# Kernel optimization log

Measured on AMD Instinct MI355X. Metric: run time of the kernel, lower is better.

The kernel has to match this reference:

```python
import jax, jax.numpy as jnp
import numpy as np

B, S, D, H = 8, 2048, 1024, 8
HD = D // H


def _linear_params(key, d_in, d_out):
    kw, kb = jax.random.split(key)
    w = jax.random.normal(kw, (d_out, d_in), jnp.float32) * 0.02
    b = jax.random.normal(kb, (d_out,), jnp.float32) * 0.02
    return w, b


def setup_inputs() -> dict:
    key = jax.random.key(0)
    ks = jax.random.split(key, 16)
    inp = {}
    inp['input_seq'] = jax.random.normal(ks[0], (B, S, D), jnp.float32)
    inp['output_seq'] = jax.random.normal(ks[1], (B, S, D), jnp.float32)
    # PositionalEncoding parameter: sin(arange(D) / 10000 ** (arange(D)/D))
    ar = jnp.arange(D, dtype=jnp.float32)
    inp['pe'] = jnp.sin(ar / 10000.0 ** (ar / D))
    names = ['enc_wq enc_bq', 'enc_wk enc_bk', 'enc_wv enc_bv',
             'enc_w1 enc_b1', 'enc_w2 enc_b2',
             'dec_s_wq dec_s_bq', 'dec_s_wk dec_s_bk', 'dec_s_wv dec_s_bv',
             'dec_c_wq dec_c_bq', 'dec_c_wk dec_c_bk', 'dec_c_wv dec_c_bv',
             'dec_w1 dec_b1', 'dec_w2 dec_b2', 'fc_w fc_b']
    for i, pair in enumerate(names):
        wn, bn = pair.split()
        w, b = _linear_params(ks[2 + i], D, D)
        inp[wn], inp[bn] = w, b
    return inp


def _mha(q_in, k_in, wq, bq, wk, bk, wv, bv):
    # Faithful to source: head split WITHOUT transpose -> per-position 8x8 head mixing.
    q = (q_in @ wq.T + bq).reshape(q_in.shape[0], q_in.shape[1], H, HD)
    k = (k_in @ wk.T + bk).reshape(k_in.shape[0], k_in.shape[1], H, HD)
    v = (k_in @ wv.T + bv).reshape(k_in.shape[0], k_in.shape[1], H, HD)
    scores = jnp.einsum('bsih,bsjh->bsij', q, k) / jnp.sqrt(jnp.float32(HD))
    w = jax.nn.softmax(scores, axis=-1)  # dropout before softmax is identity at eval
    out = jnp.einsum('bsij,bsjh->bsih', w, v)
    return out.reshape(q_in.shape[0], q_in.shape[1], -1)


def reference(input_seq, output_seq, pe,
              enc_wq, enc_bq, enc_wk, enc_bk, enc_wv, enc_bv,
              enc_w1, enc_b1, enc_w2, enc_b2,
              dec_s_wq, dec_s_bq, dec_s_wk, dec_s_bk, dec_s_wv, dec_s_bv,
              dec_c_wq, dec_c_bq, dec_c_wk, dec_c_bk, dec_c_wv, dec_c_bv,
              dec_w1, dec_b1, dec_w2, dec_b2, fc_w, fc_b):
    x = input_seq + pe  # additive positional encoding
    # encoder layer
    a = _mha(x, x, enc_wq, enc_bq, enc_wk, enc_bk, enc_wv, enc_bv)
    enc_out = jax.nn.relu(a @ enc_w1.T + enc_b1) @ enc_w2.T + enc_b2
    # decoder layer (training branch: output_seq given)
    sa = _mha(output_seq, output_seq, dec_s_wq, dec_s_bq, dec_s_wk, dec_s_bk, dec_s_wv, dec_s_bv)
    ca = _mha(sa, enc_out, dec_c_wq, dec_c_bq, dec_c_wk, dec_c_bk, dec_c_wv, dec_c_bv)
    dec_out = jax.nn.relu(ca @ dec_w1.T + dec_b1) @ dec_w2.T + dec_b2
    return dec_out @ fc_w.T + fc_b
```

## Files before the change

kernel.cpp:

```cpp
#include <hip/hip_runtime.h>
#include <stdint.h>


#define TOKENS 16384
#define DMODEL 1024

typedef unsigned short ushort_t;
typedef __attribute__((ext_vector_type(8))) short short8;
typedef __attribute__((ext_vector_type(4))) float floatx4;

__device__ __forceinline__ float b2f(ushort_t u) {
  union { uint32_t i; float f; } v; v.i = ((uint32_t)u) << 16; return v.f;
}
__device__ __forceinline__ ushort_t f2b(float f) {
  union { float f; uint32_t i; } v; v.f = f;
  uint32_t r = v.i + 0x7fffu + ((v.i >> 16) & 1u);
  return (ushort_t)(r >> 16);
}

__device__ __forceinline__ void pack8(const float* __restrict__ g, ushort_t* dst) {
  float4 x = *(const float4*)g;
  float4 y = *(const float4*)(g + 4);
  ushort_t o[8] = {f2b(x.x), f2b(x.y), f2b(x.z), f2b(x.w),
                   f2b(y.x), f2b(y.y), f2b(y.z), f2b(y.w)};
  *(uint4*)dst = *(uint4*)o;
}

#define GLD16(g, l)                                                          \
  __builtin_amdgcn_global_load_lds(                                          \
      (const __attribute__((address_space(1))) void*)(g),                    \
      (__attribute__((address_space(3))) void*)(l), 16, 0, 0)

struct ConvArgs {
  const float* src[14];
  ushort_t* dst[14];
};

__global__ __launch_bounds__(256) void conv_w_kernel(ConvArgs a) {
  const int w = blockIdx.y;
  const int idx = (blockIdx.x * 256 + threadIdx.x) * 8;
  pack8(a.src[w] + idx, a.dst[w] + idx);
}

__global__ __launch_bounds__(256) void conv_x_kernel(
    const float* __restrict__ src, ushort_t* __restrict__ dst) {
  const int idx = (blockIdx.x * 256 + threadIdx.x) * 8;
  pack8(src + idx, dst + idx);
}

__global__ __launch_bounds__(256) void add_pe_kernel(
    const float* __restrict__ in, const float* __restrict__ pe,
    ushort_t* __restrict__ out) {
  int idx = (blockIdx.x * 256 + threadIdx.x) * 8;
  int d = idx & (DMODEL - 1);
  float4 a0 = *(const float4*)(in + idx);
  float4 a1 = *(const float4*)(in + idx + 4);
  float4 p0 = *(const float4*)(pe + d);
  float4 p1 = *(const float4*)(pe + d + 4);
  ushort_t o[8] = {f2b(a0.x + p0.x), f2b(a0.y + p0.y), f2b(a0.z + p0.z), f2b(a0.w + p0.w),
                   f2b(a1.x + p1.x), f2b(a1.y + p1.y), f2b(a1.z + p1.z), f2b(a1.w + p1.w)};
  *(uint4*)(out + idx) = *(uint4*)o;
}

__device__ __forceinline__ void load_af(const ushort_t* p, int aoff, int cs0,
                                        int cs1, short8 (&af)[4][2]) {
  p += aoff;
#pragma unroll
  for (int i = 0; i < 4; i++) {
    af[i][0] = *(const short8*)&p[i * 1024 + cs0];
    af[i][1] = *(const short8*)&p[i * 1024 + cs1];
  }
}

__device__ __forceinline__ void load_bf(const ushort_t* p, int boff, int cs0,
                                        int cs1, short8 (&bf)[2][2]) {
  p += boff;
#pragma unroll
  for (int j = 0; j < 2; j++) {
    bf[j][0] = *(const short8*)&p[j * 1024 + cs0];
    bf[j][1] = *(const short8*)&p[j * 1024 + cs1];
  }
}

template <int QA, int QB>
__device__ __forceinline__ void mfma_region(floatx4 (&acc)[4][4][2],
                                            const short8 (&af)[4][2],
                                            const short8 (&b0)[2][2],
                                            const short8 (&b1)[2][2]) {
  __builtin_amdgcn_s_setprio(1);
#pragma unroll
  for (int i = 0; i < 4; i++)
#pragma unroll
    for (int j = 0; j < 2; j++) {
      acc[QA][i][j] = __builtin_amdgcn_mfma_f32_16x16x32_bf16(
          af[i][0], b0[j][0], acc[QA][i][j], 0, 0, 0);
      acc[QA][i][j] = __builtin_amdgcn_mfma_f32_16x16x32_bf16(
          af[i][1], b0[j][1], acc[QA][i][j], 0, 0, 0);
    }
#pragma unroll
  for (int i = 0; i < 4; i++)
#pragma unroll
    for (int j = 0; j < 2; j++) {
      acc[QB][i][j] = __builtin_amdgcn_mfma_f32_16x16x32_bf16(
          af[i][0], b1[j][0], acc[QB][i][j], 0, 0, 0);
      acc[QB][i][j] = __builtin_amdgcn_mfma_f32_16x16x32_bf16(
          af[i][1], b1[j][1], acc[QB][i][j], 0, 0, 0);
    }
  __builtin_amdgcn_s_setprio(0);
}

#define BARSB asm volatile("s_barrier" ::: "memory")

#define STAGE_A4(dst, tk)                                                    \
  do {                                                                       \
    GLD16(gA + (size_t)(tk) * 64, (dst) + lo);                               \
    GLD16(gA + (size_t)(tk) * 64 + 65536, (dst) + 4096 + lo);                \
    GLD16(gA + (size_t)(tk) * 64 + 131072, (dst) + 8192 + lo);               \
    GLD16(gA + (size_t)(tk) * 64 + 196608, (dst) + 12288 + lo);              \
  } while (0)
#define STAGE_B4(dst, tk)                                                    \
  do {                                                                       \
    GLD16(gB + (size_t)(tk) * 64, (dst) + lo);                               \
    GLD16(gB + (size_t)(tk) * 64 + 65536, (dst) + 4096 + lo);                \
    GLD16(gB + (size_t)(tk) * 64 + 131072, (dst) + 8192 + lo);               \
    GLD16(gB + (size_t)(tk) * 64 + 196608, (dst) + 12288 + lo);              \
  } while (0)

template <bool RELU, bool OUT32>
__global__ __launch_bounds__(512, 2) void gemm_bt(
    const ushort_t* __restrict__ A, const ushort_t* __restrict__ W,
    const float* __restrict__ bias, void* __restrict__ Cp) {
  constexpr int K = 1024, N = 1024, NT = 16;
  extern __shared__ ushort_t smem[];
  ushort_t* sA = smem;
  ushort_t* sB = smem + 49152;

  const int tid = threadIdx.x;
  const int lane = tid & 63;
  const int wid = tid >> 6;

  const int orig = blockIdx.x;
  const int swz = (orig & 7) * 32 + (orig >> 3);
  const int m0 = (swz >> 2) * 256;
  const int n0 = (swz & 3) * 256;

  const int qm = (wid >> 2) * 64;
  const int qn = (wid & 3) * 32;
  const int lr = lane & 15;
  const int lq = lane >> 4;
  const int xr = lane & 7;
  const int cs0 = (lq ^ xr) * 8;
  const int cs1 = ((4 + lq) ^ xr) * 8;
  const int aoff = (qm + lr) * 64;
  const int boff = (qn + lr) * 64;

  const int rl = tid >> 3;
  const int j8 = tid & 7;
  const int co = (j8 ^ (rl & 7)) * 8;
  const int lo = tid * 8;
  const ushort_t* gA = A + (size_t)(m0 + rl) * K + co;
  const ushort_t* gB = W + (size_t)(n0 + rl) * K + co;

  floatx4 acc[4][4][2] = {};
  short8 af[4][2], bf0[2][2], bf1[2][2];

  STAGE_A4(sA, 0);
  STAGE_B4(sB, 0);
  STAGE_A4(sA + 16384, 1);
  asm volatile("s_waitcnt vmcnt(4)" ::: "memory");
  BARSB;

  int ba = 0;
#pragma unroll 1
  for (int t = 0; t < NT; ++t) {
    const ushort_t* sAb = sA + ba * 16384;
    const ushort_t* sBb = sB + (t & 1) * 16384;
    int ba2 = ba + 2; if (ba2 >= 3) ba2 -= 3;
    ushort_t* sAs = sA + ba2 * 16384;
    ushort_t* sBs = sB + ((t + 1) & 1) * 16384;

    if (t + 1 < NT) STAGE_B4(sBs, t + 1);
    if (t + 2 < NT) STAGE_A4(sAs, t + 2);

    load_af(sAb, aoff, cs0, cs1, af);
    load_bf(sBb, boff, cs0, cs1, bf0);
    load_bf(sBb + 8192, boff, cs0, cs1, bf1);
    mfma_region<0, 1>(acc, af, bf0, bf1);
    load_af(sAb + 8192, aoff, cs0, cs1, af);
    mfma_region<2, 3>(acc, af, bf0, bf1);

    if (t + 2 < NT)
      asm volatile("s_waitcnt vmcnt(4)" ::: "memory");
    else
      asm volatile("s_waitcnt vmcnt(0)" ::: "memory");
    BARSB;

    ba = (ba == 2) ? 0 : ba + 1;
  }

  const int rbase = lq * 4;

  if constexpr (OUT32) {
    float* sCf = (float*)smem;
#pragma unroll
    for (int p = 0; p < 4; p++) {
      if ((qm >> 6) == (p & 1)) {
#pragma unroll
        for (int Nh = 0; Nh < 2; Nh++)
#pragma unroll
          for (int j = 0; j < 2; j++) {
            const int col = Nh * 128 + qn + j * 16 + lr;
            const float bv = bias[n0 + col];
#pragma unroll
            for (int i = 0; i < 4; i++)
#pragma unroll
              for (int r = 0; r < 4; r++) {
                float v = acc[(p >> 1) * 2 + Nh][i][j][r] + bv;
                if (RELU) v = fmaxf(v, 0.0f);
                sCf[(i * 16 + rbase + r) * 260 + col] = v;
              }
          }
      }
      __syncthreads();
#pragma unroll
      for (int u = 0; u < 8; u++) {
        const int lin = u * 512 + tid;
        const int row = lin >> 6;
        const int c4 = (lin & 63) * 4;
        *(float4*)((float*)Cp + (size_t)(m0 + p * 64 + row) * N + n0 + c4) =
            *(const float4*)&sCf[row * 260 + c4];
      }
      __syncthreads();
    }
    return;
  }

  ushort_t* sC = smem;
#pragma unroll
  for (int p = 0; p < 2; p++) {
#pragma unroll
    for (int Nh = 0; Nh < 2; Nh++)
#pragma unroll
      for (int j = 0; j < 2; j++) {
        const int col = Nh * 128 + qn + j * 16 + lr;
        const float bv = bias[n0 + col];
#pragma unroll
        for (int i = 0; i < 4; i++)
#pragma unroll
          for (int r = 0; r < 4; r++) {
            float v = acc[p * 2 + Nh][i][j][r] + bv;
            if (RELU) v = fmaxf(v, 0.0f);
            sC[(qm + i * 16 + rbase + r) * 264 + col] = f2b(v);
          }
      }
    __syncthreads();
#pragma unroll
    for (int u = 0; u < 8; u++) {
      const int lin = u * 512 + tid;
      const int row = lin >> 5;
      const int c8 = (lin & 31) * 8;
      *(uint4*)((ushort_t*)Cp + (size_t)(m0 + p * 128 + row) * N + n0 + c8) =
          *(const uint4*)&sC[row * 264 + c8];
    }
    __syncthreads();
  }
}

__global__ __launch_bounds__(256) void attn_kernel(
    const ushort_t* Q, const ushort_t* Kp, const ushort_t* Vp, ushort_t* O) {
  __shared__ __align__(16) ushort_t sq[4][1024];
  __shared__ __align__(16) ushort_t sk[4][1024];
  __shared__ __align__(16) ushort_t sv[4][1024];
  __shared__ float sp[4][64];

  const int t = threadIdx.x;
  const int w = t >> 6;
  const int lane = t & 63;
  const size_t base = ((size_t)blockIdx.x * 4 + w) * 1024;

  ((uint4*)sq[w])[lane] = ((const uint4*)(Q + base))[lane];
  ((uint4*)sq[w])[lane + 64] = ((const uint4*)(Q + base))[lane + 64];
  ((uint4*)sk[w])[lane] = ((const uint4*)(Kp + base))[lane];
  ((uint4*)sk[w])[lane + 64] = ((const uint4*)(Kp + base))[lane + 64];
  ((uint4*)sv[w])[lane] = ((const uint4*)(Vp + base))[lane];
  ((uint4*)sv[w])[lane + 64] = ((const uint4*)(Vp + base))[lane + 64];
  __syncthreads();

  {
    const int i = lane >> 3, j = lane & 7;
    const ushort_t* qr = &sq[w][i * 128];
    const ushort_t* kr = &sk[w][j * 128];
    float s = 0.0f;
#pragma unroll 16
    for (int h = 0; h < 128; h++) s += b2f(qr[h]) * b2f(kr[h]);
    s *= 0.08838834764831845f;
    float m = s;
#pragma unroll
    for (int off = 1; off < 8; off <<= 1) m = fmaxf(m, __shfl_xor(m, off, 64));
    float e = __expf(s - m);
    float sum = e;
#pragma unroll
    for (int off = 1; off < 8; off <<= 1) sum += __shfl_xor(sum, off, 64);
    sp[w][lane] = e / sum;
  }
  __syncthreads();

  {
    const int i = lane >> 3;
    const int hb = (lane & 7) * 16;
    float p[8];
#pragma unroll
    for (int jj = 0; jj < 8; jj++) p[jj] = sp[w][i * 8 + jj];
    float o[16];
#pragma unroll
    for (int h = 0; h < 16; h++) {
      float acc = 0.0f;
#pragma unroll
      for (int jj = 0; jj < 8; jj++) acc += p[jj] * b2f(sv[w][jj * 128 + hb + h]);
      o[h] = acc;
    }
    uint32_t packed[8];
#pragma unroll
    for (int u = 0; u < 8; u++)
      packed[u] = (uint32_t)f2b(o[2 * u]) | ((uint32_t)f2b(o[2 * u + 1]) << 16);
    uint4* dst = (uint4*)(O + base + i * 128 + hb);
    dst[0] = *(uint4*)&packed[0];
    dst[1] = *(uint4*)&packed[4];
  }
}

extern "C" void kernel_launch(void* const* d_in, const int* in_sizes, int n_in,
                              void* d_out, int out_size, void* d_ws, size_t ws_size,
                              hipStream_t stream) {
  const float* input_seq = (const float*)d_in[0];
  const float* output_seq = (const float*)d_in[1];
  const float* pe = (const float*)d_in[2];
  const float* wsrc[14] = {
      (const float*)d_in[3],  (const float*)d_in[5],  (const float*)d_in[7],
      (const float*)d_in[9],  (const float*)d_in[11], (const float*)d_in[13],
      (const float*)d_in[15], (const float*)d_in[17], (const float*)d_in[19],
      (const float*)d_in[21], (const float*)d_in[23], (const float*)d_in[25],
      (const float*)d_in[27], (const float*)d_in[29]};
  const float* enc_bq = (const float*)d_in[4];
  const float* enc_bk = (const float*)d_in[6];
  const float* enc_bv = (const float*)d_in[8];
  const float* enc_b1 = (const float*)d_in[10];
  const float* enc_b2 = (const float*)d_in[12];
  const float* dsq_b = (const float*)d_in[14];
  const float* dsk_b = (const float*)d_in[16];
  const float* dsv_b = (const float*)d_in[18];
  const float* dcq_b = (const float*)d_in[20];
  const float* dck_b = (const float*)d_in[22];
  const float* dcv_b = (const float*)d_in[24];
  const float* dec_b1 = (const float*)d_in[26];
  const float* dec_b2 = (const float*)d_in[28];
  const float* fc_b = (const float*)d_in[30];

  const size_t SZ = (size_t)TOKENS * DMODEL;
  const size_t WSZ = (size_t)DMODEL * DMODEL;
  ushort_t* bA = (ushort_t*)d_ws;
  ushort_t* bB = bA + SZ;
  ushort_t* oseq = bB + SZ;
  ushort_t* wts = oseq + SZ;
  ushort_t* oL = (ushort_t*)d_out;
  ushort_t* oH = oL + SZ;
  float* outf = (float*)d_out;

  static bool attr_set = false;
  if (!attr_set) {
    (void)hipFuncSetAttribute(reinterpret_cast<const void*>(&gemm_bt<false, false>),
                              hipFuncAttributeMaxDynamicSharedMemorySize, 163840);
    (void)hipFuncSetAttribute(reinterpret_cast<const void*>(&gemm_bt<true, false>),
                              hipFuncAttributeMaxDynamicSharedMemorySize, 163840);
    (void)hipFuncSetAttribute(reinterpret_cast<const void*>(&gemm_bt<false, true>),
                              hipFuncAttributeMaxDynamicSharedMemorySize, 163840);
    attr_set = true;
  }

  ConvArgs ca;
#pragma unroll
  for (int i = 0; i < 14; i++) { ca.src[i] = wsrc[i]; ca.dst[i] = wts + (size_t)i * WSZ; }

  const dim3 gG(TOKENS / 256 * (DMODEL / 256));
  const dim3 gblk(512);
  const dim3 blk(256);
  const int LDSB = 163840;
  const int gPE = TOKENS * DMODEL / (256 * 8);
  const int gAT = TOKENS / 4;

  conv_w_kernel<<<dim3(WSZ / (256 * 8), 14), blk, 0, stream>>>(ca);
  conv_x_kernel<<<gPE, blk, 0, stream>>>(output_seq, oseq);
  add_pe_kernel<<<gPE, blk, 0, stream>>>(input_seq, pe, bA);
  gemm_bt<false, false><<<gG, gblk, LDSB, stream>>>(bA, wts + 0 * WSZ, enc_bq, bB);
  gemm_bt<false, false><<<gG, gblk, LDSB, stream>>>(bA, wts + 1 * WSZ, enc_bk, oL);
  gemm_bt<false, false><<<gG, gblk, LDSB, stream>>>(bA, wts + 2 * WSZ, enc_bv, oH);
  attn_kernel<<<gAT, blk, 0, stream>>>(bB, oL, oH, bB);
  gemm_bt<true, false><<<gG, gblk, LDSB, stream>>>(bB, wts + 3 * WSZ, enc_b1, bA);
  gemm_bt<false, false><<<gG, gblk, LDSB, stream>>>(bA, wts + 4 * WSZ, enc_b2, bB);
  gemm_bt<false, false><<<gG, gblk, LDSB, stream>>>(oseq, wts + 5 * WSZ, dsq_b, bA);
  gemm_bt<false, false><<<gG, gblk, LDSB, stream>>>(oseq, wts + 6 * WSZ, dsk_b, oL);
  gemm_bt<false, false><<<gG, gblk, LDSB, stream>>>(oseq, wts + 7 * WSZ, dsv_b, oH);
  attn_kernel<<<gAT, blk, 0, stream>>>(bA, oL, oH, bA);
  gemm_bt<false, false><<<gG, gblk, LDSB, stream>>>(bA, wts + 8 * WSZ, dcq_b, oL);
  gemm_bt<false, false><<<gG, gblk, LDSB, stream>>>(bB, wts + 9 * WSZ, dck_b, oH);
  gemm_bt<false, false><<<gG, gblk, LDSB, stream>>>(bB, wts + 10 * WSZ, dcv_b, bA);
  attn_kernel<<<gAT, blk, 0, stream>>>(oL, oH, bA, oL);
  gemm_bt<true, false><<<gG, gblk, LDSB, stream>>>(oL, wts + 11 * WSZ, dec_b1, bB);
  gemm_bt<false, false><<<gG, gblk, LDSB, stream>>>(bB, wts + 12 * WSZ, dec_b2, bA);
  gemm_bt<false, true><<<gG, gblk, LDSB, stream>>>(bA, wts + 13 * WSZ, fc_b, outf);
}
```

Measured before the change: 845.0 us.

## Restructure GEMM main loop into 8-wave ping-pong schedule with double buffering

Replaces the triple-buffered A / double-buffered B pipeline with a double-buffered scheme. Each K tile is split into four quadrant MFMA phases separated by barriers, and LDS fragment loads and the next tile's global staging are interleaved between phases. The next tile's fragments are prefetched into alternating register sets. LDS use drops from 160KB to 128KB. The extra barriers per tile and the full vmcnt(0) wait could stall if global loads are not hidden, though the intent is tighter overlap of LDS reads with MFMA.

```diff
diff --git a/kernel.cpp b/kernel.cpp
--- a/kernel.cpp
+++ b/kernel.cpp
@@ -82,29 +82,18 @@
   }
 }
 
-template <int QA, int QB>
-__device__ __forceinline__ void mfma_region(floatx4 (&acc)[4][4][2],
-                                            const short8 (&af)[4][2],
-                                            const short8 (&b0)[2][2],
-                                            const short8 (&b1)[2][2]) {
+__device__ __forceinline__ void mfma_q(floatx4 (&accq)[4][2],
+                                       const short8 (&af)[4][2],
+                                       const short8 (&bf)[2][2]) {
   __builtin_amdgcn_s_setprio(1);
 #pragma unroll
   for (int i = 0; i < 4; i++)
 #pragma unroll
     for (int j = 0; j < 2; j++) {
-      acc[QA][i][j] = __builtin_amdgcn_mfma_f32_16x16x32_bf16(
-          af[i][0], b0[j][0], acc[QA][i][j], 0, 0, 0);
-      acc[QA][i][j] = __builtin_amdgcn_mfma_f32_16x16x32_bf16(
-          af[i][1], b0[j][1], acc[QA][i][j], 0, 0, 0);
-    }
-#pragma unroll
-  for (int i = 0; i < 4; i++)
-#pragma unroll
-    for (int j = 0; j < 2; j++) {
-      acc[QB][i][j] = __builtin_amdgcn_mfma_f32_16x16x32_bf16(
-          af[i][0], b1[j][0], acc[QB][i][j], 0, 0, 0);
-      acc[QB][i][j] = __builtin_amdgcn_mfma_f32_16x16x32_bf16(
-          af[i][1], b1[j][1], acc[QB][i][j], 0, 0, 0);
+      accq[i][j] = __builtin_amdgcn_mfma_f32_16x16x32_bf16(
+          af[i][0], bf[j][0], accq[i][j], 0, 0, 0);
+      accq[i][j] = __builtin_amdgcn_mfma_f32_16x16x32_bf16(
+          af[i][1], bf[j][1], accq[i][j], 0, 0, 0);
     }
   __builtin_amdgcn_s_setprio(0);
 }
@@ -126,6 +115,33 @@
     GLD16(gB + (size_t)(tk) * 64 + 196608, (dst) + 12288 + lo);              \
   } while (0)
 
+#define GROUP(tt, dd, b0c, b0n)                                              \
+  do {                                                                       \
+                                                                     \
+    if ((tt) + 1 < NT) {                                                     \
+      STAGE_A4(sA + ((dd) ^ 1) * 16384, (tt) + 1);                           \
+      STAGE_B4(sB + ((dd) ^ 1) * 16384, (tt) + 1);                           \
+    }                                                                        \
+    load_bf(sB + (dd) * 16384 + 8192, boff, cs0, cs1, b1);                   \
+    BARSB;                                                                   \
+    mfma_q(acc[0], atop, b0c);                                               \
+                                                                     \
+    load_af(sA + (dd) * 16384 + 8192, aoff, cs0, cs1, abot);                 \
+    BARSB;                                                                   \
+    mfma_q(acc[1], atop, b1);                                                \
+                                                                     \
+    asm volatile("s_waitcnt vmcnt(0)" ::: "memory");                         \
+    BARSB;                                                                   \
+    mfma_q(acc[3], abot, b1);                                                \
+                                                                     \
+    if ((tt) + 1 < NT) {                                                     \
+      load_af(sA + ((dd) ^ 1) * 16384, aoff, cs0, cs1, atop);                \
+      load_bf(sB + ((dd) ^ 1) * 16384, boff, cs0, cs1, b0n);                 \
+    }                                                                        \
+    BARSB;                                                                   \
+    mfma_q(acc[2], abot, b0c);                                               \
+  } while (0)
+
 template <bool RELU, bool OUT32>
 __global__ __launch_bounds__(512, 2) void gemm_bt(
     const ushort_t* __restrict__ A, const ushort_t* __restrict__ W,
@@ -133,7 +149,7 @@
   constexpr int K = 1024, N = 1024, NT = 16;
   extern __shared__ ushort_t smem[];
   ushort_t* sA = smem;
-  ushort_t* sB = smem + 49152;
+  ushort_t* sB = smem + 32768;
 
   const int tid = threadIdx.x;
   const int lane = tid & 63;
@@ -162,40 +178,19 @@
   const ushort_t* gB = W + (size_t)(n0 + rl) * K + co;
 
   floatx4 acc[4][4][2] = {};
-  short8 af[4][2], bf0[2][2], bf1[2][2];
+  short8 atop[4][2], abot[4][2], b0E[2][2], b0O[2][2], b1[2][2];
 
   STAGE_A4(sA, 0);
   STAGE_B4(sB, 0);
-  STAGE_A4(sA + 16384, 1);
-  asm volatile("s_waitcnt vmcnt(4)" ::: "memory");
+  asm volatile("s_waitcnt vmcnt(0)" ::: "memory");
   BARSB;
-
-  int ba = 0;
+  load_af(sA, aoff, cs0, cs1, atop);
+  load_bf(sB, boff, cs0, cs1, b0E);
+
 #pragma unroll 1
-  for (int t = 0; t < NT; ++t) {
-    const ushort_t* sAb = sA + ba * 16384;
-    const ushort_t* sBb = sB + (t & 1) * 16384;
-    int ba2 = ba + 2; if (ba2 >= 3) ba2 -= 3;
-    ushort_t* sAs = sA + ba2 * 16384;
-    ushort_t* sBs = sB + ((t + 1) & 1) * 16384;
-
-    if (t + 1 < NT) STAGE_B4(sBs, t + 1);
-    if (t + 2 < NT) STAGE_A4(sAs, t + 2);
-
-    load_af(sAb, aoff, cs0, cs1, af);
-    load_bf(sBb, boff, cs0, cs1, bf0);
-    load_bf(sBb + 8192, boff, cs0, cs1, bf1);
-    mfma_region<0, 1>(acc, af, bf0, bf1);
-    load_af(sAb + 8192, aoff, cs0, cs1, af);
-    mfma_region<2, 3>(acc, af, bf0, bf1);
-
-    if (t + 2 < NT)
-      asm volatile("s_waitcnt vmcnt(4)" ::: "memory");
-    else
-      asm volatile("s_waitcnt vmcnt(0)" ::: "memory");
-    BARSB;
-
-    ba = (ba == 2) ? 0 : ba + 1;
+  for (int t = 0; t < NT; t += 2) {
+    GROUP(t, 0, b0E, b0O);
+    GROUP(t + 1, 1, b0O, b0E);
   }
 
   const int rbase = lq * 4;
@@ -369,11 +364,11 @@
   static bool attr_set = false;
   if (!attr_set) {
     (void)hipFuncSetAttribute(reinterpret_cast<const void*>(&gemm_bt<false, false>),
-                              hipFuncAttributeMaxDynamicSharedMemorySize, 163840);
+                              hipFuncAttributeMaxDynamicSharedMemorySize, 131072);
     (void)hipFuncSetAttribute(reinterpret_cast<const void*>(&gemm_bt<true, false>),
-                              hipFuncAttributeMaxDynamicSharedMemorySize, 163840);
+                              hipFuncAttributeMaxDynamicSharedMemorySize, 131072);
     (void)hipFuncSetAttribute(reinterpret_cast<const void*>(&gemm_bt<false, true>),
-                              hipFuncAttributeMaxDynamicSharedMemorySize, 163840);
+                              hipFuncAttributeMaxDynamicSharedMemorySize, 131072);
     attr_set = true;
   }
 
@@ -384,7 +379,7 @@
   const dim3 gG(TOKENS / 256 * (DMODEL / 256));
   const dim3 gblk(512);
   const dim3 blk(256);
-  const int LDSB = 163840;
+  const int LDSB = 131072;
   const int gPE = TOKENS * DMODEL / (256 * 8);
   const int gAT = TOKENS / 4;
 
```

After: 1.029 ms. 1.22x slower.
